# Kernel optimization log

Measured on AMD Instinct MI355X. Metric: run time of the kernel, lower is better.

## Reference

```python
import jax, jax.numpy as jnp
import numpy as np

EPS = 1e-8


def setup_inputs() -> dict:
    key = jax.random.key(0)
    ks = jax.random.split(key, 4)
    B, Cin, Cout, K, S, H, W = 16, 256, 256, 3, 512, 128, 128
    return {
        "x": jax.random.normal(ks[0], (B, Cin, H, W), dtype=jnp.float32),
        "style": jax.random.normal(ks[1], (B, S), dtype=jnp.float32),
        "weight": jax.random.normal(ks[2], (1, Cout, Cin, K, K), dtype=jnp.float32),
        "mod_w": jax.random.normal(ks[3], (Cin, S), dtype=jnp.float32) * (1.0 / np.sqrt(S)),
        "mod_b": jnp.zeros((Cin,), dtype=jnp.float32),
        "bias": jnp.zeros((1, Cout, 1, 1), dtype=jnp.float32),
    }


def reference(x, style, weight, mod_w, mod_b, bias):
    B, Cin, H, W = x.shape
    _, Cout, _, K, _ = weight.shape
    scale = 1.0 / np.sqrt(Cin * K * K)

    # modulation: Linear(style_dim -> in_channel)
    s = style @ mod_w.T + mod_b                      # [B, Cin]
    w = scale * weight * s[:, None, :, None, None]   # [B, Cout, Cin, K, K]
    demod = jax.lax.rsqrt(jnp.sum(w * w, axis=(2, 3, 4)) + EPS)  # [B, Cout]
    w = w * demod[:, :, None, None, None]

    # grouped conv with groups = batch (per-sample weights)
    w = w.reshape(B * Cout, Cin, K, K)
    xg = x.reshape(1, B * Cin, H, W)
    out = jax.lax.conv_general_dilated(
        xg, w,
        window_strides=(1, 1),
        padding=[(1, 1), (1, 1)],
        dimension_numbers=("NCHW", "OIHW", "NCHW"),
        feature_group_count=B,
    )
    Ho, Wo = out.shape[2], out.shape[3]
    out = out.reshape(B, Cout, Ho, Wo)
    return out + bias
```

## Files before the change

### kernel.cpp

```cpp
#include <hip/hip_runtime.h>
#include <stdint.h>

typedef unsigned short u16;
typedef __attribute__((ext_vector_type(8))) short short8;
typedef __attribute__((ext_vector_type(4))) float f32x4;

#define AS1 __attribute__((address_space(1)))
#define AS3 __attribute__((address_space(3)))

static __device__ __forceinline__ void gload_lds16(const void* g, void* l) {
  __builtin_amdgcn_global_load_lds((const AS1 void*)g, (AS3 void*)l, 16, 0, 0);
}

static __device__ __forceinline__ u16 bf16r(float f) {
  union { float f; uint32_t u; } c; c.f = f;
  uint32_t u = c.u;
  u += 0x7fffu + ((u >> 16) & 1u);
  return (u16)(u >> 16);
}

static constexpr int NB = 16, CIN = 256, COUT = 256, HW = 128, SDIM = 512;
static constexpr float SCALE = 1.0f / 48.0f;

__global__ void k_style(const float* __restrict__ style, const float* __restrict__ mod_w,
                        const float* __restrict__ mod_b, float* __restrict__ s) {
  int b = blockIdx.x, ci = threadIdx.x;
  const float4* st = (const float4*)(style + (size_t)b * SDIM);
  const float4* mw = (const float4*)(mod_w + (size_t)ci * SDIM);
  float acc = 0.f;
  #pragma unroll 4
  for (int j = 0; j < SDIM / 4; ++j) {
    float4 a = st[j], w = mw[j];
    acc += a.x * w.x + a.y * w.y + a.z * w.z + a.w * w.w;
  }
  s[b * CIN + ci] = acc + mod_b[ci];
}

__global__ void k_wmod(const float* __restrict__ weight, const float* __restrict__ s,
                       u16* __restrict__ Wb) {
  __shared__ float wld[CIN * 9];
  __shared__ float red[8];
  int bid = blockIdx.x;
  int b = bid >> 8, co = bid & 255;
  int t = threadIdx.x;
  const float* wsrc = weight + (size_t)co * (CIN * 9);
  for (int i = t; i < CIN * 9; i += 256) wld[i] = wsrc[i];
  __syncthreads();
  int ci = t;
  float sv = s[b * CIN + ci];
  float v[9];
  float sq = 0.f;
  #pragma unroll
  for (int k = 0; k < 9; ++k) {
    float w = SCALE * wld[ci * 9 + k] * sv;
    v[k] = w;
    sq += w * w;
  }
  #pragma unroll
  for (int off = 32; off; off >>= 1) sq += __shfl_down(sq, off);
  int lane = t & 63, wid = t >> 6;
  if (lane == 0) red[wid] = sq;
  __syncthreads();
  if (t == 0) red[4] = rsqrtf(red[0] + red[1] + red[2] + red[3] + 1e-8f);
  __syncthreads();
  float demod = red[4];
  #pragma unroll
  for (int k = 0; k < 9; ++k) {
    Wb[(((size_t)b * 9 + k) * COUT + co) * CIN + ci] = bf16r(v[k] * demod);
  }
}

__global__ void k_xt(const float* __restrict__ x, u16* __restrict__ xTp) {
  __shared__ u16 T[128 * 65];
  int bid = blockIdx.x;
  int b = bid >> 7, h = bid & 127;
  int t = threadIdx.x;
  size_t rowbase = ((size_t)b * 130 + (h + 1)) * 130 * CIN;
  xTp[rowbase + t] = 0;
  xTp[rowbase + (size_t)129 * CIN + t] = 0;
  if (h == 0) {
    uint32_t* g = (uint32_t*)(xTp + (size_t)b * 130 * 130 * CIN);
    for (int i = t; i < 130 * CIN / 2; i += 256) g[i] = 0;
  }
  if (h == 127) {
    uint32_t* g = (uint32_t*)(xTp + ((size_t)b * 130 + 129) * 130 * CIN);
    for (int i = t; i < 130 * CIN / 2; i += 256) g[i] = 0;
  }
  for (int ci0 = 0; ci0 < CIN; ci0 += 64) {
    __syncthreads();
    #pragma unroll
    for (int i = 0; i < 8; ++i) {
      int idx = t + i * 256;
      int ci = idx >> 5, px4 = idx & 31;
      float4 v = *(const float4*)(x + (((size_t)b * CIN + ci0 + ci) * HW + h) * HW + px4 * 4);
      T[(px4 * 4 + 0) * 65 + ci] = bf16r(v.x);
      T[(px4 * 4 + 1) * 65 + ci] = bf16r(v.y);
      T[(px4 * 4 + 2) * 65 + ci] = bf16r(v.z);
      T[(px4 * 4 + 3) * 65 + ci] = bf16r(v.w);
    }
    __syncthreads();
    int ci = t & 63, pxo = t >> 6;
    #pragma unroll
    for (int i = 0; i < 32; ++i) {
      int px = i * 4 + pxo;
      xTp[rowbase + (size_t)(px + 1) * CIN + ci0 + ci] = T[px * 65 + ci];
    }
  }
}

static constexpr int SLOTU = 32768;

__global__ __launch_bounds__(512, 1) void k_conv(const u16* __restrict__ Wb,
                                                 const u16* __restrict__ xTp,
                                                 const float* __restrict__ bias,
                                                 float* __restrict__ out) {
  extern __shared__ u16 lds[];
  int bid = blockIdx.x;
  int swz = (bid & 7) * 128 + (bid >> 3);
  int b = swz >> 6, hp = swz & 63;
  int h0 = hp * 2;

  int t = threadIdx.x, lane = t & 63, wid = t >> 6;
  int wr = wid >> 2, wc = wid & 3;
  int rowoff = wid * 8 + (lane >> 3);
  int swzc = ((lane & 7) ^ (lane >> 3)) << 3;
  int cxor = (lane & 7) << 3;
  int klo = (lane >> 4) << 3;
  int arow = (wr * 128 + (lane & 15)) * 64;
  int brow = (wc * 64 + (lane & 15)) * 64;
  const size_t wbB = (size_t)b * 9 * 65536;
  const size_t xB = (size_t)b * 130 * 130 * 256;

  f32x4 acc[8][4];
  #pragma unroll
  for (int i = 0; i < 8; ++i)
    #pragma unroll
    for (int j = 0; j < 4; ++j) acc[i][j] = (f32x4)0.f;

  auto srcA = [&](int kta, int i) -> const u16* {
    int kpos = kta >> 2, ci0 = (kta & 3) << 6;
    return Wb + wbB + (size_t)kpos * 65536 + (size_t)(i * 64 + rowoff) * 256 + ci0 + swzc;
  };
  auto srcB = [&](int kta, int i) -> const u16* {
    int kpos = kta >> 2, ci0 = (kta & 3) << 6;
    int kh = kpos < 3 ? 0 : (kpos < 6 ? 1 : 2);
    int kw = kpos - kh * 3;
    int hh = h0 + kh + (i >> 1);
    int pxp = kw + (i & 1) * 64 + rowoff;
    return xTp + xB + ((size_t)hh * 130 + pxp) * 256 + ci0 + swzc;
  };

  {
    u16* A2 = lds;
    u16* B2 = lds + 16384;
    #pragma unroll
    for (int i = 0; i < 4; ++i) gload_lds16(srcA(0, i), A2 + (i * 64 + wid * 8) * 64);
    #pragma unroll
    for (int i = 0; i < 4; ++i) gload_lds16(srcB(0, i), B2 + (i * 64 + wid * 8) * 64);
  }
  asm volatile("s_waitcnt vmcnt(0)" ::: "memory");
  __builtin_amdgcn_s_barrier();
  asm volatile("" ::: "memory");

  for (int kt = 0; kt < 36; ++kt) {
    u16* Ac = lds + (kt & 1) * SLOTU;
    u16* Bc = Ac + 16384;
    u16* An = lds + ((kt & 1) ^ 1) * SLOTU;
    u16* Bn = An + 16384;
    bool pf = kt < 35;
    int kta = kt + 1;

    short8 af[8], bf[4];

#define LD_A(M, KK) (*(const short8*)&Ac[arow + (M) * 1024 + (((KK) * 32 + klo) ^ cxor)])
#define LD_B(N, KK) (*(const short8*)&Bc[brow + (N) * 1024 + (((KK) * 32 + klo) ^ cxor)])

    #pragma unroll
    for (int mt = 0; mt < 8; ++mt) af[mt] = LD_A(mt, 0);
    #pragma unroll
    for (int nt = 0; nt < 4; ++nt) bf[nt] = LD_B(nt, 0);
    if (pf) {
      #pragma unroll
      for (int i = 0; i < 4; ++i) gload_lds16(srcA(kta, i), An + (i * 64 + wid * 8) * 64);
    }
    asm volatile("" ::: "memory");
    __builtin_amdgcn_s_barrier();
    asm volatile("" ::: "memory");
    __builtin_amdgcn_s_setprio(1);
    #pragma unroll
    for (int mt = 0; mt < 8; ++mt)
      #pragma unroll
      for (int nt = 0; nt < 4; ++nt)
        acc[mt][nt] = __builtin_amdgcn_mfma_f32_16x16x32_bf16(af[mt], bf[nt], acc[mt][nt], 0, 0, 0);
    __builtin_amdgcn_s_setprio(0);
    asm volatile("" ::: "memory");
    __builtin_amdgcn_s_barrier();
    asm volatile("" ::: "memory");

    #pragma unroll
    for (int mt = 0; mt < 8; ++mt) af[mt] = LD_A(mt, 1);
    #pragma unroll
    for (int nt = 0; nt < 4; ++nt) bf[nt] = LD_B(nt, 1);
    if (pf) {
      #pragma unroll
      for (int i = 0; i < 4; ++i) gload_lds16(srcB(kta, i), Bn + (i * 64 + wid * 8) * 64);
    }
    asm volatile("" ::: "memory");
    __builtin_amdgcn_s_barrier();
    asm volatile("" ::: "memory");
    __builtin_amdgcn_s_setprio(1);
    #pragma unroll
    for (int mt = 0; mt < 8; ++mt)
      #pragma unroll
      for (int nt = 0; nt < 4; ++nt)
        acc[mt][nt] = __builtin_amdgcn_mfma_f32_16x16x32_bf16(af[mt], bf[nt], acc[mt][nt], 0, 0, 0);
    __builtin_amdgcn_s_setprio(0);
    if (pf) asm volatile("s_waitcnt vmcnt(0)" ::: "memory");
    asm volatile("" ::: "memory");
    __builtin_amdgcn_s_barrier();
    asm volatile("" ::: "memory");
#undef LD_A
#undef LD_B
  }

  #pragma unroll
  for (int mt = 0; mt < 8; ++mt) {
    #pragma unroll
    for (int j = 0; j < 4; ++j) {
      int co = wr * 128 + mt * 16 + ((lane >> 4) * 4) + j;
      float bv = bias[co];
      #pragma unroll
      for (int nt = 0; nt < 4; ++nt) {
        int px = wc * 64 + nt * 16 + (lane & 15);
        int h = h0 + (px >> 7), w = px & 127;
        out[(((size_t)b * COUT + co) * HW + h) * HW + w] = acc[mt][nt][j] + bv;
      }
    }
  }
}

extern "C" void kernel_launch(void* const* d_in, const int* in_sizes, int n_in,
                              void* d_out, int out_size, void* d_ws, size_t ws_size,
                              hipStream_t stream) {
  const float* x      = (const float*)d_in[0];
  const float* style  = (const float*)d_in[1];
  const float* weight = (const float*)d_in[2];
  const float* mod_w  = (const float*)d_in[3];
  const float* mod_b  = (const float*)d_in[4];
  const float* bias   = (const float*)d_in[5];
  float* out = (float*)d_out;

  char* ws = (char*)d_ws;
  float* s   = (float*)ws;
  u16* Wb    = (u16*)(ws + 16384);
  u16* xTp   = (u16*)(ws + 16384 + (size_t)NB * 9 * COUT * CIN * 2);

  (void)hipFuncSetAttribute((const void*)k_conv,
                            hipFuncAttributeMaxDynamicSharedMemorySize, 2 * SLOTU * 2);

  k_style<<<NB, 256, 0, stream>>>(style, mod_w, mod_b, s);
  k_wmod<<<NB * COUT, 256, 0, stream>>>(weight, s, Wb);
  k_xt<<<NB * HW, 256, 0, stream>>>(x, xTp);
  k_conv<<<NB * (HW / 2), 512, 2 * SLOTU * 2, stream>>>(Wb, xTp, bias, out);
}
```

Before: 413.2 us.

## Restructure conv main loop to one barrier per step and request two blocks per CU

The per-k-step schedule drops the four explicit s_barrier points and the setprio hints. It now keeps both k-halves' fragments in separate registers: the second half's B fragments are loaded before the first MFMA batch, and A fragments after it. A single __syncthreads ends each iteration. Launch bounds are raised to request two 512-thread blocks per CU, which caps VGPRs per thread. That cap risks spilling the 128-float accumulator plus the doubled fragments, and 128 KB of LDS per block likely prevents the second block from fitting anyway.

```diff
diff --git a/kernel.cpp b/kernel.cpp
--- a/kernel.cpp
+++ b/kernel.cpp
@@ -110,7 +110,7 @@
 
 static constexpr int SLOTU = 32768;
 
-__global__ __launch_bounds__(512, 1) void k_conv(const u16* __restrict__ Wb,
+__global__ __launch_bounds__(512, 2) void k_conv(const u16* __restrict__ Wb,
                                                  const u16* __restrict__ xTp,
                                                  const float* __restrict__ bias,
                                                  float* __restrict__ out) {
@@ -158,9 +158,7 @@
     #pragma unroll
     for (int i = 0; i < 4; ++i) gload_lds16(srcB(0, i), B2 + (i * 64 + wid * 8) * 64);
   }
-  asm volatile("s_waitcnt vmcnt(0)" ::: "memory");
-  __builtin_amdgcn_s_barrier();
-  asm volatile("" ::: "memory");
+  __syncthreads();
 
   for (int kt = 0; kt < 36; ++kt) {
     u16* Ac = lds + (kt & 1) * SLOTU;
@@ -170,55 +168,37 @@
     bool pf = kt < 35;
     int kta = kt + 1;
 
-    short8 af[8], bf[4];
-
 #define LD_A(M, KK) (*(const short8*)&Ac[arow + (M) * 1024 + (((KK) * 32 + klo) ^ cxor)])
 #define LD_B(N, KK) (*(const short8*)&Bc[brow + (N) * 1024 + (((KK) * 32 + klo) ^ cxor)])
 
-    #pragma unroll
-    for (int mt = 0; mt < 8; ++mt) af[mt] = LD_A(mt, 0);
-    #pragma unroll
-    for (int nt = 0; nt < 4; ++nt) bf[nt] = LD_B(nt, 0);
+    short8 af0[8], bf0[4], af1[8], bf1[4];
+    #pragma unroll
+    for (int mt = 0; mt < 8; ++mt) af0[mt] = LD_A(mt, 0);
+    #pragma unroll
+    for (int nt = 0; nt < 4; ++nt) bf0[nt] = LD_B(nt, 0);
     if (pf) {
       #pragma unroll
       for (int i = 0; i < 4; ++i) gload_lds16(srcA(kta, i), An + (i * 64 + wid * 8) * 64);
     }
-    asm volatile("" ::: "memory");
-    __builtin_amdgcn_s_barrier();
-    asm volatile("" ::: "memory");
-    __builtin_amdgcn_s_setprio(1);
+    #pragma unroll
+    for (int nt = 0; nt < 4; ++nt) bf1[nt] = LD_B(nt, 1);
     #pragma unroll
     for (int mt = 0; mt < 8; ++mt)
       #pragma unroll
       for (int nt = 0; nt < 4; ++nt)
-        acc[mt][nt] = __builtin_amdgcn_mfma_f32_16x16x32_bf16(af[mt], bf[nt], acc[mt][nt], 0, 0, 0);
-    __builtin_amdgcn_s_setprio(0);
-    asm volatile("" ::: "memory");
-    __builtin_amdgcn_s_barrier();
-    asm volatile("" ::: "memory");
-
-    #pragma unroll
-    for (int mt = 0; mt < 8; ++mt) af[mt] = LD_A(mt, 1);
-    #pragma unroll
-    for (int nt = 0; nt < 4; ++nt) bf[nt] = LD_B(nt, 1);
+        acc[mt][nt] = __builtin_amdgcn_mfma_f32_16x16x32_bf16(af0[mt], bf0[nt], acc[mt][nt], 0, 0, 0);
     if (pf) {
       #pragma unroll
       for (int i = 0; i < 4; ++i) gload_lds16(srcB(kta, i), Bn + (i * 64 + wid * 8) * 64);
     }
-    asm volatile("" ::: "memory");
-    __builtin_amdgcn_s_barrier();
-    asm volatile("" ::: "memory");
-    __builtin_amdgcn_s_setprio(1);
+    #pragma unroll
+    for (int mt = 0; mt < 8; ++mt) af1[mt] = LD_A(mt, 1);
     #pragma unroll
     for (int mt = 0; mt < 8; ++mt)
       #pragma unroll
       for (int nt = 0; nt < 4; ++nt)
-        acc[mt][nt] = __builtin_amdgcn_mfma_f32_16x16x32_bf16(af[mt], bf[nt], acc[mt][nt], 0, 0, 0);
-    __builtin_amdgcn_s_setprio(0);
-    if (pf) asm volatile("s_waitcnt vmcnt(0)" ::: "memory");
-    asm volatile("" ::: "memory");
-    __builtin_amdgcn_s_barrier();
-    asm volatile("" ::: "memory");
+        acc[mt][nt] = __builtin_amdgcn_mfma_f32_16x16x32_bf16(af1[mt], bf1[nt], acc[mt][nt], 0, 0, 0);
+    __syncthreads();
 #undef LD_A
 #undef LD_B
   }
```

New measurement: 408.8 us. Within noise of the previous version (-1.1%).
